# Kernel optimization log

Measured on AMD Instinct MI355X. Metric: run time of the kernel, lower is better.

## Reference

```python
import jax, jax.numpy as jnp
import numpy as np

EPS_NORM = 1e-12  # matches F.normalize eps

def _l2_normalize(x):
    norm = jnp.sqrt(jnp.sum(x * x, axis=-1, keepdims=True))
    return x / jnp.maximum(norm, EPS_NORM)

def setup_inputs() -> dict:
    key = jax.random.key(0)
    k1, k2 = jax.random.split(key)
    N, C, D = 16384, 8192, 1024
    features = jax.random.normal(k1, (N, D), dtype=jnp.float32)
    # prototypes init: normal(mean=const_init=0, std=0.01)
    prototypes = 0.01 * jax.random.normal(k2, (C, D), dtype=jnp.float32)
    distance_scale = jnp.ones((1,), dtype=jnp.float32)
    return {"features": features, "prototypes": prototypes, "distance_scale": distance_scale}

def reference(features, prototypes, distance_scale):
    temperature = 1.0
    f = _l2_normalize(features)      # [N, D]
    p = _l2_normalize(prototypes)    # [C, D]
    # Both rows are unit-norm, so ||f_i - p_j||^2 = 2 - 2 f_i . p_j
    dots = jnp.einsum('nd,cd->nc', f, p)             # [N, C]
    sq = jnp.maximum(2.0 - 2.0 * dots, 1e-12)
    distances = jnp.abs(distance_scale[0]) * jnp.sqrt(sq)
    logits = -distances
    return logits / temperature
```

## Files before the change

kernel.cpp:

```cpp
#include <hip/hip_runtime.h>
#include <hip/hip_bf16.h>
#include <stdint.h>

using bf16x8 = __attribute__((ext_vector_type(8))) short;
using f32x4  = __attribute__((ext_vector_type(4))) float;

#define SBAR()   __builtin_amdgcn_s_barrier()
#define SCHED0() __builtin_amdgcn_sched_barrier(0)
#define LGKM0()  asm volatile("s_waitcnt lgkmcnt(0)" ::: "memory")
#define VM0()    asm volatile("s_waitcnt vmcnt(0)" ::: "memory")

__device__ __forceinline__ void gload_lds16(const void* g, void* l) {
  __builtin_amdgcn_global_load_lds(
      (const __attribute__((address_space(1))) void*)g,
      (__attribute__((address_space(3))) void*)l,
      16, 0, 0);
}

__device__ __forceinline__ short f2bf(float f) {
  union { float f; uint32_t u; } c; c.f = f;
  uint32_t u = c.u;
  uint32_t r = (u + 0x7fffu + ((u >> 16) & 1u)) >> 16;
  return (short)(r & 0xffffu);
}

__global__ __launch_bounds__(256) void norm_rows(
    const float* __restrict__ F, const float* __restrict__ P,
    short* __restrict__ Fb, short* __restrict__ Pb, int nF) {
  int row = blockIdx.x;
  const float* src; short* dst;
  if (row < nF) {
    src = F + (size_t)row * 1024; dst = Fb + (size_t)row * 1024;
  } else {
    int r = row - nF;
    src = P + (size_t)r * 1024; dst = Pb + (size_t)r * 1024;
  }
  int tid = threadIdx.x;
  float4 v = ((const float4*)src)[tid];
  float ss = v.x * v.x + v.y * v.y + v.z * v.z + v.w * v.w;
  #pragma unroll
  for (int off = 32; off >= 1; off >>= 1) ss += __shfl_xor(ss, off);
  __shared__ float wsum[4];
  if ((tid & 63) == 0) wsum[tid >> 6] = ss;
  __syncthreads();
  float tot = wsum[0] + wsum[1] + wsum[2] + wsum[3];
  float inv = 1.0f / fmaxf(sqrtf(tot), 1e-12f);
  short4 o;
  o.x = f2bf(v.x * inv); o.y = f2bf(v.y * inv);
  o.z = f2bf(v.z * inv); o.w = f2bf(v.w * inv);
  ((short4*)dst)[tid] = o;
}

#define BM 256
#define BN 256
#define BK 64

__global__ __launch_bounds__(512, 2) void gemm_epi(
    const short* __restrict__ A,
    const short* __restrict__ B,
    const float* __restrict__ scale,
    float* __restrict__ Out, int M, int Cc, int K) {
  __shared__ __align__(16) char smem[2 * 65536];

  const int tid  = threadIdx.x;
  const int wave = tid >> 6;
  const int lane = tid & 63;
  const int wm = wave >> 2;
  const int wn = wave & 3;
  const int hb = wn >> 1;
  const int rbB = (wn & 1) * 4;

  const int nwg = gridDim.x;
  const int cpx = nwg >> 3;
  const int swz = (blockIdx.x & 7) * cpx + (blockIdx.x >> 3);
  const int ntn = Cc / BN;
  const int tm = swz / ntn, tn = swz % ntn;

  const size_t Kb = (size_t)K * 2;
  const char* Ag = (const char*)A + (size_t)tm * BM * Kb;
  const char* Bg = (const char*)B + (size_t)tn * BN * Kb;

  int r0, c0, r1, c1;
  { int s = tid * 16;        int st = s >> 10, w = s & 1023;
    w ^= ((w >> 9) & 1) << 5; r0 = ((st >> 1) << 4) + (w >> 6); c0 = ((st & 1) << 6) + (w & 63); }
  { int s = 8192 + tid * 16; int st = s >> 10, w = s & 1023;
    w ^= ((w >> 9) & 1) << 5; r1 = ((st >> 1) << 4) + (w >> 6); c1 = ((st & 1) << 6) + (w & 63); }

  const int fr  = lane & 15;
  const int fk2 = ((lane >> 4) * 8) * 2;
  const int fragoff = fr * 64 + (fk2 ^ ((fr & 8) ? 32 : 0));

  const char* smA = smem + wm * 16384;
  const char* smB = smem + 32768 + hb * 16384;

  f32x4 acc[8][4];
  #pragma unroll
  for (int i = 0; i < 8; ++i)
    #pragma unroll
    for (int j = 0; j < 4; ++j) acc[i][j] = (f32x4){0.f, 0.f, 0.f, 0.f};

  const int nt = K / BK;

  #define STAGE(t, buf) do {                                                   \
    const size_t kb = (size_t)(t) * (BK * 2);                                  \
    char* db = smem + (buf) * 65536 + wave * 1024;                             \
    gload_lds16(Ag + (size_t)(      r0) * Kb + kb + c0, db);                   \
    gload_lds16(Ag + (size_t)(      r1) * Kb + kb + c1, db + 8192);            \
    gload_lds16(Ag + (size_t)(128 + r0) * Kb + kb + c0, db + 16384);           \
    gload_lds16(Ag + (size_t)(128 + r1) * Kb + kb + c1, db + 16384 + 8192);    \
    gload_lds16(Bg + (size_t)(      r0) * Kb + kb + c0, db + 32768);           \
    gload_lds16(Bg + (size_t)(      r1) * Kb + kb + c1, db + 32768 + 8192);    \
    gload_lds16(Bg + (size_t)(128 + r0) * Kb + kb + c0, db + 49152);           \
    gload_lds16(Bg + (size_t)(128 + r1) * Kb + kb + c1, db + 49152 + 8192);    \
  } while (0)

  #define LDA(buf, mi, ks) (*(const bf16x8*)(smA + (buf) * 65536 + ((mi) * 2 + (ks)) * 1024 + fragoff))
  #define LDB(buf, ni, ks) (*(const bf16x8*)(smB + (buf) * 65536 + ((rbB + (ni)) * 2 + (ks)) * 1024 + fragoff))

  STAGE(0, 0);
  VM0(); SCHED0(); SBAR(); SCHED0();

  for (int t = 0; t < nt; ++t) {
    const int cur = t & 1, nxt = cur ^ 1;
    if (t + 1 < nt) STAGE(t + 1, nxt);

    bf16x8 a03[4][2], b01[2][2];
    #pragma unroll
    for (int mi = 0; mi < 4; ++mi) { a03[mi][0] = LDA(cur, mi, 0); a03[mi][1] = LDA(cur, mi, 1); }
    #pragma unroll
    for (int ni = 0; ni < 2; ++ni) { b01[ni][0] = LDB(cur, ni, 0); b01[ni][1] = LDB(cur, ni, 1); }
    SBAR(); LGKM0(); SCHED0();
    __builtin_amdgcn_s_setprio(1);
    #pragma unroll
    for (int mi = 0; mi < 4; ++mi)
      #pragma unroll
      for (int ni = 0; ni < 2; ++ni) {
        acc[mi][ni] = __builtin_amdgcn_mfma_f32_16x16x32_bf16(a03[mi][0], b01[ni][0], acc[mi][ni], 0, 0, 0);
        acc[mi][ni] = __builtin_amdgcn_mfma_f32_16x16x32_bf16(a03[mi][1], b01[ni][1], acc[mi][ni], 0, 0, 0);
      }
    __builtin_amdgcn_s_setprio(0);
    SBAR(); SCHED0();

    bf16x8 b23[2][2];
    #pragma unroll
    for (int ni = 0; ni < 2; ++ni) { b23[ni][0] = LDB(cur, 2 + ni, 0); b23[ni][1] = LDB(cur, 2 + ni, 1); }
    SBAR(); LGKM0(); SCHED0();
    __builtin_amdgcn_s_setprio(1);
    #pragma unroll
    for (int mi = 0; mi < 4; ++mi)
      #pragma unroll
      for (int ni = 0; ni < 2; ++ni) {
        acc[mi][2 + ni] = __builtin_amdgcn_mfma_f32_16x16x32_bf16(a03[mi][0], b23[ni][0], acc[mi][2 + ni], 0, 0, 0);
        acc[mi][2 + ni] = __builtin_amdgcn_mfma_f32_16x16x32_bf16(a03[mi][1], b23[ni][1], acc[mi][2 + ni], 0, 0, 0);
      }
    __builtin_amdgcn_s_setprio(0);
    SBAR(); SCHED0();

    bf16x8 a47[4][2];
    #pragma unroll
    for (int mi = 0; mi < 4; ++mi) { a47[mi][0] = LDA(cur, 4 + mi, 0); a47[mi][1] = LDA(cur, 4 + mi, 1); }
    SBAR(); LGKM0(); SCHED0();
    __builtin_amdgcn_s_setprio(1);
    #pragma unroll
    for (int mi = 0; mi < 4; ++mi)
      #pragma unroll
      for (int ni = 0; ni < 2; ++ni) {
        acc[4 + mi][2 + ni] = __builtin_amdgcn_mfma_f32_16x16x32_bf16(a47[mi][0], b23[ni][0], acc[4 + mi][2 + ni], 0, 0, 0);
        acc[4 + mi][2 + ni] = __builtin_amdgcn_mfma_f32_16x16x32_bf16(a47[mi][1], b23[ni][1], acc[4 + mi][2 + ni], 0, 0, 0);
      }
    __builtin_amdgcn_s_setprio(0);
    SBAR(); SCHED0();

    bf16x8 b01b[2][2];
    #pragma unroll
    for (int ni = 0; ni < 2; ++ni) { b01b[ni][0] = LDB(cur, ni, 0); b01b[ni][1] = LDB(cur, ni, 1); }
    SBAR(); LGKM0(); SCHED0();
    __builtin_amdgcn_s_setprio(1);
    #pragma unroll
    for (int mi = 0; mi < 4; ++mi)
      #pragma unroll
      for (int ni = 0; ni < 2; ++ni) {
        acc[4 + mi][ni] = __builtin_amdgcn_mfma_f32_16x16x32_bf16(a47[mi][0], b01b[ni][0], acc[4 + mi][ni], 0, 0, 0);
        acc[4 + mi][ni] = __builtin_amdgcn_mfma_f32_16x16x32_bf16(a47[mi][1], b01b[ni][1], acc[4 + mi][ni], 0, 0, 0);
      }
    __builtin_amdgcn_s_setprio(0);
    VM0(); SCHED0();
    SBAR(); SCHED0();
  }

  const float sc = fabsf(scale[0]);
  const int orow0 = tm * BM + wm * 128 + (lane >> 4) * 4;
  const int ocol0 = tn * BN + wn * 64 + fr;
  #pragma unroll
  for (int mi = 0; mi < 8; ++mi) {
    #pragma unroll
    for (int ni = 0; ni < 4; ++ni) {
      const int col = ocol0 + ni * 16;
      #pragma unroll
      for (int r = 0; r < 4; ++r) {
        float d  = acc[mi][ni][r];
        float sq = fmaxf(2.0f - 2.0f * d, 1e-12f);
        __builtin_nontemporal_store(-sc * sqrtf(sq),
            &Out[(size_t)(orow0 + mi * 16 + r) * Cc + col]);
      }
    }
  }
  #undef STAGE
  #undef LDA
  #undef LDB
}

extern "C" void kernel_launch(void* const* d_in, const int* in_sizes, int n_in,
                              void* d_out, int out_size, void* d_ws, size_t ws_size,
                              hipStream_t stream) {
  const float* F = (const float*)d_in[0];
  const float* P = (const float*)d_in[1];
  const float* S = (const float*)d_in[2];
  float* Out = (float*)d_out;

  const int D = 1024;
  const int N = in_sizes[0] / D;
  const int C = in_sizes[1] / D;

  short* Fb = (short*)d_ws;
  short* Pb = Fb + (size_t)N * D;

  norm_rows<<<N + C, 256, 0, stream>>>(F, P, Fb, Pb, N);

  dim3 grid((N / BM) * (C / BN));
  gemm_epi<<<grid, 512, 0, stream>>>(Fb, Pb, S, Out, N, C, D);
}
```

Baseline: 845.4 us.

## Split tile prefetch into quarter stages with partial vmcnt waits

Breaks each K-tile's global-to-LDS prefetch into four chunks (B low, B high, A even, A odd). Each chunk is issued just before the quadrant of MFMAs that needs it. The loop is unrolled by two so the buffer indices are compile-time constants. Partial vmcnt waits replace the full drain at the end of each iteration, so later loads can stay in flight while earlier quadrants compute. The risk is extra barrier-ordering complexity and a possible race if the chunk ordering and wait counts do not match the LDS reads.

New measurement: 820.8 us. 2.9% less time.

```diff
diff --git a/kernel.cpp b/kernel.cpp
--- a/kernel.cpp
+++ b/kernel.cpp
@@ -8,7 +8,7 @@
 #define SBAR()   __builtin_amdgcn_s_barrier()
 #define SCHED0() __builtin_amdgcn_sched_barrier(0)
 #define LGKM0()  asm volatile("s_waitcnt lgkmcnt(0)" ::: "memory")
-#define VM0()    asm volatile("s_waitcnt vmcnt(0)" ::: "memory")
+#define VMW(n)   asm volatile("s_waitcnt vmcnt(" #n ")" ::: "memory")
 
 __device__ __forceinline__ void gload_lds16(const void* g, void* l) {
   __builtin_amdgcn_global_load_lds(
@@ -99,92 +99,109 @@
     #pragma unroll
     for (int j = 0; j < 4; ++j) acc[i][j] = (f32x4){0.f, 0.f, 0.f, 0.f};
 
-  const int nt = K / BK;
-
-  #define STAGE(t, buf) do {                                                   \
-    const size_t kb = (size_t)(t) * (BK * 2);                                  \
+  #define STG_BLO(t, buf) do { const size_t kb = (size_t)(t) * (BK * 2);       \
+    char* db = smem + (buf) * 65536 + wave * 1024;                             \
+    gload_lds16(Bg + (size_t)(      r0) * Kb + kb + c0, db + 32768);           \
+    gload_lds16(Bg + (size_t)(      r1) * Kb + kb + c1, db + 40960); } while (0)
+  #define STG_BHI(t, buf) do { const size_t kb = (size_t)(t) * (BK * 2);       \
+    char* db = smem + (buf) * 65536 + wave * 1024;                             \
+    gload_lds16(Bg + (size_t)(128 + r0) * Kb + kb + c0, db + 49152);           \
+    gload_lds16(Bg + (size_t)(128 + r1) * Kb + kb + c1, db + 57344); } while (0)
+  #define STG_AEV(t, buf) do { const size_t kb = (size_t)(t) * (BK * 2);       \
     char* db = smem + (buf) * 65536 + wave * 1024;                             \
     gload_lds16(Ag + (size_t)(      r0) * Kb + kb + c0, db);                   \
+    gload_lds16(Ag + (size_t)(128 + r0) * Kb + kb + c0, db + 16384); } while (0)
+  #define STG_AOD(t, buf) do { const size_t kb = (size_t)(t) * (BK * 2);       \
+    char* db = smem + (buf) * 65536 + wave * 1024;                             \
     gload_lds16(Ag + (size_t)(      r1) * Kb + kb + c1, db + 8192);            \
-    gload_lds16(Ag + (size_t)(128 + r0) * Kb + kb + c0, db + 16384);           \
-    gload_lds16(Ag + (size_t)(128 + r1) * Kb + kb + c1, db + 16384 + 8192);    \
-    gload_lds16(Bg + (size_t)(      r0) * Kb + kb + c0, db + 32768);           \
-    gload_lds16(Bg + (size_t)(      r1) * Kb + kb + c1, db + 32768 + 8192);    \
-    gload_lds16(Bg + (size_t)(128 + r0) * Kb + kb + c0, db + 49152);           \
-    gload_lds16(Bg + (size_t)(128 + r1) * Kb + kb + c1, db + 49152 + 8192);    \
-  } while (0)
+    gload_lds16(Ag + (size_t)(128 + r1) * Kb + kb + c1, db + 24576); } while (0)
 
   #define LDA(buf, mi, ks) (*(const bf16x8*)(smA + (buf) * 65536 + ((mi) * 2 + (ks)) * 1024 + fragoff))
-  #define LDB(buf, ni, ks) (*(const bf16x8*)(smB + (buf) * 65536 + ((rbB + (ni)) * 2 + (ks)) * 1024 + fragoff))
-
-  STAGE(0, 0);
-  VM0(); SCHED0(); SBAR(); SCHED0();
-
-  for (int t = 0; t < nt; ++t) {
-    const int cur = t & 1, nxt = cur ^ 1;
-    if (t + 1 < nt) STAGE(t + 1, nxt);
-
-    bf16x8 a03[4][2], b01[2][2];
-    #pragma unroll
-    for (int mi = 0; mi < 4; ++mi) { a03[mi][0] = LDA(cur, mi, 0); a03[mi][1] = LDA(cur, mi, 1); }
-    #pragma unroll
-    for (int ni = 0; ni < 2; ++ni) { b01[ni][0] = LDB(cur, ni, 0); b01[ni][1] = LDB(cur, ni, 1); }
-    SBAR(); LGKM0(); SCHED0();
-    __builtin_amdgcn_s_setprio(1);
-    #pragma unroll
-    for (int mi = 0; mi < 4; ++mi)
-      #pragma unroll
-      for (int ni = 0; ni < 2; ++ni) {
-        acc[mi][ni] = __builtin_amdgcn_mfma_f32_16x16x32_bf16(a03[mi][0], b01[ni][0], acc[mi][ni], 0, 0, 0);
-        acc[mi][ni] = __builtin_amdgcn_mfma_f32_16x16x32_bf16(a03[mi][1], b01[ni][1], acc[mi][ni], 0, 0, 0);
-      }
-    __builtin_amdgcn_s_setprio(0);
-    SBAR(); SCHED0();
-
-    bf16x8 b23[2][2];
-    #pragma unroll
-    for (int ni = 0; ni < 2; ++ni) { b23[ni][0] = LDB(cur, 2 + ni, 0); b23[ni][1] = LDB(cur, 2 + ni, 1); }
-    SBAR(); LGKM0(); SCHED0();
-    __builtin_amdgcn_s_setprio(1);
-    #pragma unroll
-    for (int mi = 0; mi < 4; ++mi)
-      #pragma unroll
-      for (int ni = 0; ni < 2; ++ni) {
-        acc[mi][2 + ni] = __builtin_amdgcn_mfma_f32_16x16x32_bf16(a03[mi][0], b23[ni][0], acc[mi][2 + ni], 0, 0, 0);
-        acc[mi][2 + ni] = __builtin_amdgcn_mfma_f32_16x16x32_bf16(a03[mi][1], b23[ni][1], acc[mi][2 + ni], 0, 0, 0);
-      }
-    __builtin_amdgcn_s_setprio(0);
-    SBAR(); SCHED0();
-
-    bf16x8 a47[4][2];
-    #pragma unroll
-    for (int mi = 0; mi < 4; ++mi) { a47[mi][0] = LDA(cur, 4 + mi, 0); a47[mi][1] = LDA(cur, 4 + mi, 1); }
-    SBAR(); LGKM0(); SCHED0();
-    __builtin_amdgcn_s_setprio(1);
-    #pragma unroll
-    for (int mi = 0; mi < 4; ++mi)
-      #pragma unroll
-      for (int ni = 0; ni < 2; ++ni) {
-        acc[4 + mi][2 + ni] = __builtin_amdgcn_mfma_f32_16x16x32_bf16(a47[mi][0], b23[ni][0], acc[4 + mi][2 + ni], 0, 0, 0);
-        acc[4 + mi][2 + ni] = __builtin_amdgcn_mfma_f32_16x16x32_bf16(a47[mi][1], b23[ni][1], acc[4 + mi][2 + ni], 0, 0, 0);
-      }
-    __builtin_amdgcn_s_setprio(0);
-    SBAR(); SCHED0();
-
-    bf16x8 b01b[2][2];
-    #pragma unroll
-    for (int ni = 0; ni < 2; ++ni) { b01b[ni][0] = LDB(cur, ni, 0); b01b[ni][1] = LDB(cur, ni, 1); }
-    SBAR(); LGKM0(); SCHED0();
-    __builtin_amdgcn_s_setprio(1);
-    #pragma unroll
-    for (int mi = 0; mi < 4; ++mi)
-      #pragma unroll
-      for (int ni = 0; ni < 2; ++ni) {
-        acc[4 + mi][ni] = __builtin_amdgcn_mfma_f32_16x16x32_bf16(a47[mi][0], b01b[ni][0], acc[4 + mi][ni], 0, 0, 0);
-        acc[4 + mi][ni] = __builtin_amdgcn_mfma_f32_16x16x32_bf16(a47[mi][1], b01b[ni][1], acc[4 + mi][ni], 0, 0, 0);
-      }
-    __builtin_amdgcn_s_setprio(0);
-    VM0(); SCHED0();
+  #define LDB(buf, nj, ks) (*(const bf16x8*)(smB + (buf) * 65536 + ((rbB + (nj)) * 2 + (ks)) * 1024 + fragoff))
+
+  #define RD_A(AR, buf, mbase)                                                 \
+    _Pragma("unroll")                                                          \
+    for (int mi = 0; mi < 4; ++mi) {                                           \
+      AR[mi][0] = LDA(buf, (mbase) + mi, 0);                                   \
+      AR[mi][1] = LDA(buf, (mbase) + mi, 1); }
+  #define RD_B(BR, buf, nbase)                                                 \
+    _Pragma("unroll")                                                          \
+    for (int nj = 0; nj < 2; ++nj) {                                           \
+      BR[nj][0] = LDB(buf, (nbase) + nj, 0);                                   \
+      BR[nj][1] = LDB(buf, (nbase) + nj, 1); }
+  #define MFMA_Q(mbase, nbase, AR, BR)                                         \
+    _Pragma("unroll")                                                          \
+    for (int mi = 0; mi < 4; ++mi)                                             \
+      _Pragma("unroll")                                                        \
+      for (int nj = 0; nj < 2; ++nj) {                                         \
+        acc[(mbase)+mi][(nbase)+nj] = __builtin_amdgcn_mfma_f32_16x16x32_bf16( \
+            AR[mi][0], BR[nj][0], acc[(mbase)+mi][(nbase)+nj], 0, 0, 0);       \
+        acc[(mbase)+mi][(nbase)+nj] = __builtin_amdgcn_mfma_f32_16x16x32_bf16( \
+            AR[mi][1], BR[nj][1], acc[(mbase)+mi][(nbase)+nj], 0, 0, 0); }
+
+  const int ni = K / (2 * BK);
+
+  STG_BLO(0, 0); STG_BHI(0, 0); STG_AEV(0, 0); STG_AOD(0, 0); SCHED0();
+  VMW(2); SCHED0(); SBAR(); SCHED0();
+
+  for (int i = 0; i < ni; ++i) {
+    const int t1 = 2 * i + 1;
+    const int t2 = 2 * i + 2;
+    const bool last = (i == ni - 1);
+
+    bf16x8 a03[4][2], a47[4][2], bA[2][2], bB[2][2];
+
+    RD_A(a03, 0, 0); RD_B(bA, 0, 0);
+    STG_BLO(t1, 1); SCHED0();
+    SBAR(); LGKM0(); SCHED0();
+    __builtin_amdgcn_s_setprio(1); MFMA_Q(0, 0, a03, bA) __builtin_amdgcn_s_setprio(0);
+    SBAR(); SCHED0();
+
+    RD_B(bB, 0, 2);
+    STG_BHI(t1, 1); SCHED0();
+    SBAR(); LGKM0(); SCHED0();
+    __builtin_amdgcn_s_setprio(1); MFMA_Q(0, 2, a03, bB) __builtin_amdgcn_s_setprio(0);
+    VMW(4); SCHED0();
+    SBAR(); SCHED0();
+
+    RD_A(a47, 0, 4);
+    STG_AEV(t1, 1); SCHED0();
+    SBAR(); LGKM0(); SCHED0();
+    __builtin_amdgcn_s_setprio(1); MFMA_Q(4, 2, a47, bB) __builtin_amdgcn_s_setprio(0);
+    SBAR(); SCHED0();
+
+    RD_B(bA, 0, 0);
+    STG_AOD(t1, 1); SCHED0();
+    SBAR(); LGKM0(); SCHED0();
+    __builtin_amdgcn_s_setprio(1); MFMA_Q(4, 0, a47, bA) __builtin_amdgcn_s_setprio(0);
+    VMW(2); SCHED0();
+    SBAR(); SCHED0();
+
+    RD_A(a03, 1, 0); RD_B(bA, 1, 0);
+    if (!last) { STG_BLO(t2, 0); } SCHED0();
+    SBAR(); LGKM0(); SCHED0();
+    __builtin_amdgcn_s_setprio(1); MFMA_Q(0, 0, a03, bA) __builtin_amdgcn_s_setprio(0);
+    SBAR(); SCHED0();
+
+    RD_B(bB, 1, 2);
+    if (!last) { STG_BHI(t2, 0); } SCHED0();
+    SBAR(); LGKM0(); SCHED0();
+    __builtin_amdgcn_s_setprio(1); MFMA_Q(0, 2, a03, bB) __builtin_amdgcn_s_setprio(0);
+    if (!last) { VMW(4); } else { VMW(0); }
+    SCHED0();
+    SBAR(); SCHED0();
+
+    RD_A(a47, 1, 4);
+    if (!last) { STG_AEV(t2, 0); } SCHED0();
+    SBAR(); LGKM0(); SCHED0();
+    __builtin_amdgcn_s_setprio(1); MFMA_Q(4, 2, a47, bB) __builtin_amdgcn_s_setprio(0);
+    SBAR(); SCHED0();
+
+    RD_B(bA, 1, 0);
+    if (!last) { STG_AOD(t2, 0); } SCHED0();
+    SBAR(); LGKM0(); SCHED0();
+    __builtin_amdgcn_s_setprio(1); MFMA_Q(4, 0, a47, bA) __builtin_amdgcn_s_setprio(0);
+    VMW(2); SCHED0();
     SBAR(); SCHED0();
   }
 
@@ -194,20 +211,17 @@
   #pragma unroll
   for (int mi = 0; mi < 8; ++mi) {
     #pragma unroll
-    for (int ni = 0; ni < 4; ++ni) {
-      const int col = ocol0 + ni * 16;
+    for (int nj = 0; nj < 4; ++nj) {
+      const int col = ocol0 + nj * 16;
       #pragma unroll
       for (int r = 0; r < 4; ++r) {
-        float d  = acc[mi][ni][r];
+        float d  = acc[mi][nj][r];
         float sq = fmaxf(2.0f - 2.0f * d, 1e-12f);
         __builtin_nontemporal_store(-sc * sqrtf(sq),
             &Out[(size_t)(orow0 + mi * 16 + r) * Cc + col]);
       }
     }
   }
-  #undef STAGE
-  #undef LDA
-  #undef LDB
 }
 
 extern "C" void kernel_launch(void* const* d_in, const int* in_sizes, int n_in,
```
